# Optimization experiments

Hardware: AMD Instinct MI355X
Metric: run time of the kernel (lower is better)

Reference implementation:

```python
import jax, jax.numpy as jnp
import numpy as np

B, T, D, M = 4, 4096, 2048, 512


def setup_inputs() -> dict:
    key = jax.random.key(0)
    ks = jax.random.split(key, 6)
    x = jax.random.normal(ks[0], (B, T, D), dtype=jnp.float32)
    memory_state = jnp.zeros((B, M), dtype=jnp.float32)
    # xavier_normal-style init for the linear layers, zero biases
    Wv = jax.random.normal(ks[1], (M, D), dtype=jnp.float32) * np.float32(np.sqrt(2.0 / (D + M)))
    bv = jnp.zeros((M,), dtype=jnp.float32)
    Wg = jax.random.normal(ks[2], (D, D + M), dtype=jnp.float32) * np.float32(np.sqrt(2.0 / (2 * D + M)))
    bg = jnp.zeros((D,), dtype=jnp.float32)
    time_decay = jax.random.normal(ks[3], (M,), dtype=jnp.float32) * 0.01
    time_first = jax.random.normal(ks[4], (M,), dtype=jnp.float32) * 0.01
    return dict(x=x, memory_state=memory_state, Wv=Wv, bv=bv, Wg=Wg, bg=bg,
                time_decay=time_decay, time_first=time_first)


def reference(x, memory_state, Wv, bv, Wg, bg, time_decay, time_first):
    # v = value_proj(x): [B, T, M]
    v = jnp.einsum('btd,md->btm', x, Wv) + bv
    decay = jax.nn.sigmoid(time_decay) * 0.9 + 0.1   # [M]
    first = jax.nn.sigmoid(time_first)               # [M]

    # Recurrence: s_0 = memory_state; wv_t = v_t + s_t*first; s_{t+1} = s_t*decay + v_t
    def step(s, v_t):
        wv_t = v_t + s * first
        return s * decay + v_t, wv_t

    v_tb = jnp.swapaxes(v, 0, 1)                     # [T, B, M] for scan over time
    next_memory, wv_tb = jax.lax.scan(step, memory_state, v_tb)
    weighted_values = jnp.swapaxes(wv_tb, 0, 1)      # [B, T, M]

    # output = x + output_gate(concat[x, weighted_values])
    combined = jnp.concatenate([x, weighted_values], axis=-1)  # [B, T, D+M]
    output = x + jnp.einsum('btk,dk->btd', combined, Wg) + bg
    return output, next_memory
```

## Files before the change

kernel.cpp:

```cpp
#include <hip/hip_runtime.h>
#include <hip/hip_bf16.h>
#include <cstdint>
#include <cstddef>

#define B_DIM 4
#define T_DIM 4096
#define D_DIM 2048
#define M_DIM 512
#define NTOK  (B_DIM * T_DIM)
#define KCOMB (D_DIM + M_DIM)
#define NCHUNK 64
#define CLEN   64

typedef __attribute__((ext_vector_type(8)))  __bf16 bf16x8;
typedef __attribute__((ext_vector_type(16))) float  f32x16;

__device__ __forceinline__ unsigned short f2bf(float f) {
  union { float f; unsigned u; } v; v.f = f;
  unsigned r = v.u + 0x7fffu + ((v.u >> 16) & 1u);
  return (unsigned short)(r >> 16);
}

__device__ __forceinline__ float sigmoidf(float x) { return 1.0f / (1.0f + expf(-x)); }

#define XBLK  ((NTOK * D_DIM / 4) / 256)
#define WVBLK ((M_DIM * D_DIM / 4) / 256)
#define WGBLK ((D_DIM * KCOMB / 4) / 256)
__global__ void cast_all_kernel(const float* __restrict__ x, const float* __restrict__ Wv,
                                const float* __restrict__ Wg,
                                unsigned short* __restrict__ comb,
                                unsigned short* __restrict__ WvB,
                                unsigned short* __restrict__ WgB) {
  int bid = blockIdx.x;
  const float* src; unsigned short* dst; size_t soff, doff;
  if (bid < XBLK) {
    int idx = bid * 256 + threadIdx.x;
    int n = idx >> 9;
    int c = (idx & 511) << 2;
    src = x;   soff = (size_t)n * D_DIM + c;
    dst = comb; doff = (size_t)n * KCOMB + c;
  } else if (bid < XBLK + WVBLK) {
    int idx = (bid - XBLK) * 256 + threadIdx.x;
    src = Wv;  soff = (size_t)idx * 4;
    dst = WvB; doff = (size_t)idx * 4;
  } else {
    int idx = (bid - XBLK - WVBLK) * 256 + threadIdx.x;
    src = Wg;  soff = (size_t)idx * 4;
    dst = WgB; doff = (size_t)idx * 4;
  }
  float4 v = *(const float4*)(src + soff);
  ushort4 o;
  o.x = f2bf(v.x); o.y = f2bf(v.y); o.z = f2bf(v.z); o.w = f2bf(v.w);
  *(ushort4*)(dst + doff) = o;
}

__global__ __launch_bounds__(M_DIM) void recur_partial(
    const float* __restrict__ v, const float* __restrict__ td, float* __restrict__ P) {
  int m = threadIdx.x;
  int b = blockIdx.x >> 6;
  int c = blockIdx.x & (NCHUNK - 1);
  float decay = sigmoidf(td[m]) * 0.9f + 0.1f;
  const float* vp = v + ((size_t)(b * T_DIM + c * CLEN)) * M_DIM + m;
  float p = 0.0f;
  for (int t0 = 0; t0 < CLEN; t0 += 8) {
    float vt[8];
#pragma unroll
    for (int u = 0; u < 8; ++u) vt[u] = vp[(size_t)(t0 + u) * M_DIM];
#pragma unroll
    for (int u = 0; u < 8; ++u) p = p * decay + vt[u];
  }
  P[(size_t)blockIdx.x * M_DIM + m] = p;
}

__global__ __launch_bounds__(M_DIM) void recur_apply(
    const float* __restrict__ v, const float* __restrict__ mem0,
    const float* __restrict__ td, const float* __restrict__ tf,
    const float* __restrict__ P,
    unsigned short* __restrict__ comb, float* __restrict__ nmem) {
  int m = threadIdx.x;
  int b = blockIdx.x >> 6;
  int c = blockIdx.x & (NCHUNK - 1);
  float decay = sigmoidf(td[m]) * 0.9f + 0.1f;
  float first = sigmoidf(tf[m]);
  float dL = decay;
  dL = dL * dL; dL = dL * dL; dL = dL * dL; dL = dL * dL; dL = dL * dL; dL = dL * dL;

  float s = mem0[b * M_DIM + m];
  const float* Pp = P + (size_t)(b * NCHUNK) * M_DIM + m;
  for (int ci = 0; ci < c; ++ci)
    s = s * dL + Pp[(size_t)ci * M_DIM];

  const float* vp = v + ((size_t)(b * T_DIM + c * CLEN)) * M_DIM + m;
  unsigned short* wp = comb + ((size_t)(b * T_DIM + c * CLEN)) * KCOMB + D_DIM + m;
  for (int t0 = 0; t0 < CLEN; t0 += 8) {
    float vt[8];
#pragma unroll
    for (int u = 0; u < 8; ++u) vt[u] = vp[(size_t)(t0 + u) * M_DIM];
#pragma unroll
    for (int u = 0; u < 8; ++u) {
      wp[(size_t)(t0 + u) * KCOMB] = f2bf(vt[u] + s * first);
      s = s * decay + vt[u];
    }
  }
  if (c == NCHUNK - 1) nmem[b * M_DIM + m] = s;
}

#define BM 128
#define BN 128
#define BK 64

template <bool ADD_X, int MODE>
__global__ __launch_bounds__(256) void gemm_bt(
    const unsigned short* __restrict__ A, int lda,
    const unsigned short* __restrict__ B, int ldb,
    const float* __restrict__ bias, const float* __restrict__ xadd,
    float* __restrict__ C, int N, int K) {
  const int tid = threadIdx.x;
  const int lane = tid & 63;
  const int wave = tid >> 6;
  const int wm = (wave >> 1) * 64;
  const int wn = (wave & 1) * 64;
  const int l31 = lane & 31;
  const int half = lane >> 5;

  int tileM, tileN;
  {
    int idx = blockIdx.x;
    int xcd = idx & 7, local = idx >> 3;
    if (MODE == 1) {
      tileN = (xcd * 2 + (local & 1)) * BN;
      tileM = (local >> 1) * BM;
    } else {
      tileM = (xcd * 16 + (local >> 2)) * BM;
      tileN = (local & 3) * BN;
    }
  }

  __shared__ unsigned short As[BM * BK];
  __shared__ unsigned short Bs[BN * BK];

  f32x16 acc[2][2] = {};

  for (int k0 = 0; k0 < K; k0 += BK) {
#pragma unroll
    for (int j = 0; j < 4; ++j) {
      int c = j * 256 + tid;
      int row = c >> 3;
      int kc = c & 7;
      int gkc = kc ^ (row & 7);
      const unsigned short* gA = A + (size_t)(tileM + row) * lda + k0 + gkc * 8;
      const unsigned short* gB = B + (size_t)(tileN + row) * ldb + k0 + gkc * 8;
      __builtin_amdgcn_global_load_lds((const __attribute__((address_space(1))) void*)gA,
                                       (__attribute__((address_space(3))) void*)(As + c * 8),
                                       16, 0, 0);
      __builtin_amdgcn_global_load_lds((const __attribute__((address_space(1))) void*)gB,
                                       (__attribute__((address_space(3))) void*)(Bs + c * 8),
                                       16, 0, 0);
    }
    __syncthreads();

#pragma unroll
    for (int s = 0; s < 4; ++s) {
      const int g = s * 2 + half;
      bf16x8 af[2], bfr[2];
#pragma unroll
      for (int i = 0; i < 2; ++i) {
        int ra = wm + i * 32 + l31;
        int rb = wn + i * 32 + l31;
        af[i]  = *(const bf16x8*)(As + ra * BK + ((g ^ (ra & 7)) * 8));
        bfr[i] = *(const bf16x8*)(Bs + rb * BK + ((g ^ (rb & 7)) * 8));
      }
#pragma unroll
      for (int mi = 0; mi < 2; ++mi)
#pragma unroll
        for (int ni = 0; ni < 2; ++ni)
          acc[mi][ni] = __builtin_amdgcn_mfma_f32_32x32x16_bf16(af[mi], bfr[ni], acc[mi][ni], 0, 0, 0);
    }
    __syncthreads();
  }

#pragma unroll
  for (int mi = 0; mi < 2; ++mi) {
#pragma unroll
    for (int ni = 0; ni < 2; ++ni) {
      int col = tileN + wn + ni * 32 + l31;
      float bcol = bias[col];
#pragma unroll
      for (int r = 0; r < 16; ++r) {
        int row = tileM + wm + mi * 32 + 4 * half + (r & 3) + 8 * (r >> 2);
        float val = acc[mi][ni][r] + bcol;
        if (ADD_X) val += xadd[(size_t)row * N + col];
        C[(size_t)row * N + col] = val;
      }
    }
  }
}

#define BAR_FENCE() do { asm volatile("" ::: "memory"); \
  __builtin_amdgcn_s_barrier(); asm volatile("" ::: "memory"); } while (0)

template <bool ADD_X, int LDA, int LDB, int NOUT, int KTOT>
__global__ __launch_bounds__(512, 2) void gemm256_bt(
    const unsigned short* __restrict__ Amat,
    const unsigned short* __restrict__ Bmat,
    const float* __restrict__ bias,
    const float* __restrict__ xadd,
    float* __restrict__ C) {
  constexpr int NK  = KTOT / 64;
  constexpr int NI  = NK / 2;
  constexpr int NTN = NOUT / 256;
  constexpr int NWG = (NTOK / 256) * NTN;
  constexpr int PERX = NWG / 8;

  __shared__ unsigned short As[2][256 * 64];
  __shared__ unsigned short Bs[2][256 * 64];

  const int tid  = threadIdx.x;
  const int lane = tid & 63;
  const int half = lane >> 5;
  const int l31  = lane & 31;
  const int wave = tid >> 6;
  const int wrow = (wave >> 2) * 128;
  const int wcol = (wave & 3) * 64;

  const int bid   = blockIdx.x;
  const int wgid  = (bid & 7) * PERX + (bid >> 3);
  const int tileM = (wgid / NTN) * 256;
  const int tileN = (wgid % NTN) * 256;

  const int row_lo = tid >> 3;
  const int scol   = (((tid & 7) ^ (row_lo & 7)) << 3);
  const unsigned short* pA = Amat + (size_t)(tileM + row_lo) * LDA + scol;
  const unsigned short* pB = Bmat + (size_t)(tileN + row_lo) * LDB + scol;

#define STAGE_A(b, h, kt) do { \
  _Pragma("unroll") for (int j = 0; j < 2; ++j) { \
    const unsigned short* _s = pA + (size_t)((h) * 128 + j * 64) * LDA + (kt) * 64; \
    __builtin_amdgcn_global_load_lds((const __attribute__((address_space(1))) void*)_s, \
        (__attribute__((address_space(3))) void*)(&As[(b)][(h) * 8192 + (j * 512 + tid) * 8]), \
        16, 0, 0); \
  } \
} while (0)

#define STAGE_B(b, h, kt) do { \
  _Pragma("unroll") for (int j = 0; j < 2; ++j) { \
    const unsigned short* _s = pB + (size_t)((h) * 128 + j * 64) * LDB + (kt) * 64; \
    __builtin_amdgcn_global_load_lds((const __attribute__((address_space(1))) void*)_s, \
        (__attribute__((address_space(3))) void*)(&Bs[(b)][(h) * 8192 + (j * 512 + tid) * 8]), \
        16, 0, 0); \
  } \
} while (0)

  f32x16 acc[4][2] = {};
  bf16x8 af[2][4];
  bf16x8 bfr[4];

#define READ_A(b, mh) do { \
  _Pragma("unroll") for (int mi = 0; mi < 2; ++mi) { \
    const int _r = wrow + (mh) * 64 + mi * 32 + l31; \
    _Pragma("unroll") for (int s = 0; s < 4; ++s) \
      af[mi][s] = *(const bf16x8*)(&As[(b)][_r * 64 + (((s * 2 + half) ^ (_r & 7)) << 3)]); \
  } \
} while (0)

#define READ_B(b, ni) do { \
  const int _r = wcol + (ni) * 32 + l31; \
  _Pragma("unroll") for (int s = 0; s < 4; ++s) \
    bfr[s] = *(const bf16x8*)(&Bs[(b)][_r * 64 + (((s * 2 + half) ^ (_r & 7)) << 3)]); \
} while (0)

#define MFMA_QUAD(mh, ni) do { \
  _Pragma("unroll") for (int s = 0; s < 4; ++s) \
    _Pragma("unroll") for (int mi = 0; mi < 2; ++mi) \
      acc[(mh) * 2 + mi][(ni)] = __builtin_amdgcn_mfma_f32_32x32x16_bf16( \
          af[mi][s], bfr[s], acc[(mh) * 2 + mi][(ni)], 0, 0, 0); \
} while (0)

#define PHASE_TAIL(mh, ni) do { \
  BAR_FENCE(); \
  asm volatile("s_waitcnt lgkmcnt(0)" ::: "memory"); \
  __builtin_amdgcn_s_setprio(1); \
  MFMA_QUAD(mh, ni); \
  __builtin_amdgcn_s_setprio(0); \
  BAR_FENCE(); \
} while (0)

  STAGE_A(0, 0, 0);
  STAGE_A(0, 1, 0);
  STAGE_B(0, 0, 0);
  STAGE_B(0, 1, 0);
  STAGE_A(1, 0, 1);
  asm volatile("s_waitcnt vmcnt(2)" ::: "memory");
  BAR_FENCE();

#define ITER8(KE, FULL) do { \
   \
  READ_A(0, 0); READ_B(0, 0); \
  STAGE_A(1, 1, (KE) + 1); \
  asm volatile("s_waitcnt lgkmcnt(8)" ::: "memory"); \
  PHASE_TAIL(0, 0); \
   \
  READ_B(0, 1); \
  STAGE_B(1, 0, (KE) + 1); \
  PHASE_TAIL(0, 1); \
   \
  READ_A(0, 1); \
  STAGE_B(1, 1, (KE) + 1); \
  PHASE_TAIL(1, 1); \
   \
  READ_B(0, 0); \
  if (FULL) { STAGE_A(0, 0, (KE) + 2); \
              asm volatile("s_waitcnt vmcnt(2)" ::: "memory"); } \
  else      { asm volatile("s_waitcnt vmcnt(0)" ::: "memory"); } \
  PHASE_TAIL(1, 0); \
   \
  READ_A(1, 0); READ_B(1, 0); \
  if (FULL) STAGE_A(0, 1, (KE) + 2); \
  asm volatile("s_waitcnt lgkmcnt(8)" ::: "memory"); \
  PHASE_TAIL(0, 0); \
   \
  READ_B(1, 1); \
  if (FULL) STAGE_B(0, 0, (KE) + 2); \
  PHASE_TAIL(0, 1); \
   \
  READ_A(1, 1); \
  if (FULL) STAGE_B(0, 1, (KE) + 2); \
  PHASE_TAIL(1, 1); \
   \
  READ_B(1, 0); \
  if (FULL) { STAGE_A(1, 0, (KE) + 3); \
              asm volatile("s_waitcnt vmcnt(2)" ::: "memory"); } \
  PHASE_TAIL(1, 0); \
} while (0)

#pragma unroll 1
  for (int i = 0; i < NI - 1; ++i) ITER8(2 * i, 1);
  ITER8(2 * (NI - 1), 0);

#undef ITER8
#undef PHASE_TAIL
#undef MFMA_QUAD
#undef READ_B
#undef READ_A
#undef STAGE_B
#undef STAGE_A

#pragma unroll
  for (int mq = 0; mq < 4; ++mq) {
#pragma unroll
    for (int ni = 0; ni < 2; ++ni) {
      const int col = tileN + wcol + ni * 32 + l31;
      const float bc = bias[col];
#pragma unroll
      for (int r = 0; r < 16; ++r) {
        const int row = tileM + wrow + mq * 32 + 4 * half + (r & 3) + 8 * (r >> 2);
        float val = acc[mq][ni][r] + bc;
        if (ADD_X) val += xadd[(size_t)row * NOUT + col];
        C[(size_t)row * NOUT + col] = val;
      }
    }
  }
}

extern "C" void kernel_launch(void* const* d_in, const int* in_sizes, int n_in,
                              void* d_out, int out_size, void* d_ws, size_t ws_size,
                              hipStream_t stream) {
  const float* x   = (const float*)d_in[0];
  const float* mem = (const float*)d_in[1];
  const float* Wv  = (const float*)d_in[2];
  const float* bv  = (const float*)d_in[3];
  const float* Wg  = (const float*)d_in[4];
  const float* bg  = (const float*)d_in[5];
  const float* td  = (const float*)d_in[6];
  const float* tf  = (const float*)d_in[7];
  float* out = (float*)d_out;

  char* ws = (char*)d_ws;
  unsigned short* comb = (unsigned short*)ws;
  float* v = (float*)(ws + (size_t)NTOK * KCOMB * 2);
  unsigned short* WvB = (unsigned short*)((char*)v + (size_t)NTOK * M_DIM * 4);
  unsigned short* WgB = (unsigned short*)((char*)WvB + (size_t)M_DIM * D_DIM * 2);
  float* P = (float*)WvB;

  cast_all_kernel<<<XBLK + WVBLK + WGBLK, 256, 0, stream>>>(x, Wv, Wg, comb, WvB, WgB);

  gemm_bt<false, 0><<<(NTOK / BM) * (M_DIM / BN), 256, 0, stream>>>(
      comb, KCOMB, WvB, D_DIM, bv, nullptr, v, M_DIM, D_DIM);

  recur_partial<<<B_DIM * NCHUNK, M_DIM, 0, stream>>>(v, td, P);
  recur_apply<<<B_DIM * NCHUNK, M_DIM, 0, stream>>>(
      v, mem, td, tf, P, comb, out + (size_t)NTOK * D_DIM);

  gemm256_bt<true, KCOMB, KCOMB, D_DIM, KCOMB>
      <<<(NTOK / 256) * (D_DIM / 256), 512, 0, stream>>>(comb, WgB, bg, x, out);
}
```

Baseline: 512.3 us.

## Split B fragments by k-subslice and restage global loads in pairs

Restructures the GEMM main loop so each phase reads B fragments for both N sub-tiles over half the K slice, and runs MFMAs across mi×ni rather than over the full K for one ni. Global-to-LDS staging is regrouped so that whole A or B buffers are issued together, with vmcnt thresholds adjusted to match. A sched_barrier is added before the MFMA block. The aim is better interleaving of LDS reads, global loads and MFMA issue. The risk is a mismatch between the new staging order and the waits, or extra register pressure.

```diff
diff --git a/kernel.cpp b/kernel.cpp
--- a/kernel.cpp
+++ b/kernel.cpp
@@ -253,7 +253,7 @@
 
   f32x16 acc[4][2] = {};
   bf16x8 af[2][4];
-  bf16x8 bfr[4];
+  bf16x8 bfr[2][2];
 
 #define READ_A(b, mh) do { \
   _Pragma("unroll") for (int mi = 0; mi < 2; ++mi) { \
@@ -263,84 +263,81 @@
   } \
 } while (0)
 
-#define READ_B(b, ni) do { \
-  const int _r = wcol + (ni) * 32 + l31; \
-  _Pragma("unroll") for (int s = 0; s < 4; ++s) \
-    bfr[s] = *(const bf16x8*)(&Bs[(b)][_r * 64 + (((s * 2 + half) ^ (_r & 7)) << 3)]); \
-} while (0)
-
-#define MFMA_QUAD(mh, ni) do { \
-  _Pragma("unroll") for (int s = 0; s < 4; ++s) \
+#define READ_BSP(b, sp) do { \
+  _Pragma("unroll") for (int ni = 0; ni < 2; ++ni) { \
+    const int _r = wcol + ni * 32 + l31; \
+    _Pragma("unroll") for (int j = 0; j < 2; ++j) \
+      bfr[ni][j] = *(const bf16x8*)(&Bs[(b)][_r * 64 + \
+          (((((sp) * 2 + j) * 2 + half) ^ (_r & 7)) << 3)]); \
+  } \
+} while (0)
+
+#define MFMA_Q(mh, sp) do { \
+  _Pragma("unroll") for (int j = 0; j < 2; ++j) \
     _Pragma("unroll") for (int mi = 0; mi < 2; ++mi) \
-      acc[(mh) * 2 + mi][(ni)] = __builtin_amdgcn_mfma_f32_32x32x16_bf16( \
-          af[mi][s], bfr[s], acc[(mh) * 2 + mi][(ni)], 0, 0, 0); \
-} while (0)
-
-#define PHASE_TAIL(mh, ni) do { \
+      _Pragma("unroll") for (int ni = 0; ni < 2; ++ni) \
+        acc[(mh) * 2 + mi][(ni)] = __builtin_amdgcn_mfma_f32_32x32x16_bf16( \
+            af[mi][(sp) * 2 + j], bfr[ni][j], acc[(mh) * 2 + mi][(ni)], 0, 0, 0); \
+} while (0)
+
+#define PHASE_TAIL(mh, sp) do { \
   BAR_FENCE(); \
   asm volatile("s_waitcnt lgkmcnt(0)" ::: "memory"); \
+  __builtin_amdgcn_sched_barrier(0); \
   __builtin_amdgcn_s_setprio(1); \
-  MFMA_QUAD(mh, ni); \
+  MFMA_Q(mh, sp); \
   __builtin_amdgcn_s_setprio(0); \
   BAR_FENCE(); \
 } while (0)
 
-  STAGE_A(0, 0, 0);
-  STAGE_A(0, 1, 0);
-  STAGE_B(0, 0, 0);
-  STAGE_B(0, 1, 0);
-  STAGE_A(1, 0, 1);
-  asm volatile("s_waitcnt vmcnt(2)" ::: "memory");
+  STAGE_A(0, 0, 0); STAGE_A(0, 1, 0);
+  STAGE_B(0, 0, 0); STAGE_B(0, 1, 0);
+  STAGE_A(1, 0, 1); STAGE_A(1, 1, 1);
+  asm volatile("s_waitcnt vmcnt(4)" ::: "memory");
   BAR_FENCE();
 
-#define ITER8(KE, FULL) do { \
-   \
-  READ_A(0, 0); READ_B(0, 0); \
-  STAGE_A(1, 1, (KE) + 1); \
-  asm volatile("s_waitcnt lgkmcnt(8)" ::: "memory"); \
+#define ITER(i2, FULL) do { \
+   \
+  READ_A(0, 0); READ_BSP(0, 0); \
+  STAGE_B(1, 0, (i2) + 1); STAGE_B(1, 1, (i2) + 1); \
   PHASE_TAIL(0, 0); \
    \
-  READ_B(0, 1); \
-  STAGE_B(1, 0, (KE) + 1); \
+  READ_BSP(0, 1); \
   PHASE_TAIL(0, 1); \
    \
   READ_A(0, 1); \
-  STAGE_B(1, 1, (KE) + 1); \
   PHASE_TAIL(1, 1); \
    \
-  READ_B(0, 0); \
-  if (FULL) { STAGE_A(0, 0, (KE) + 2); \
-              asm volatile("s_waitcnt vmcnt(2)" ::: "memory"); } \
+  READ_BSP(0, 0); \
+  if (FULL) { STAGE_A(0, 0, (i2) + 2); STAGE_A(0, 1, (i2) + 2); \
+              asm volatile("s_waitcnt vmcnt(4)" ::: "memory"); } \
   else      { asm volatile("s_waitcnt vmcnt(0)" ::: "memory"); } \
   PHASE_TAIL(1, 0); \
    \
-  READ_A(1, 0); READ_B(1, 0); \
-  if (FULL) STAGE_A(0, 1, (KE) + 2); \
-  asm volatile("s_waitcnt lgkmcnt(8)" ::: "memory"); \
+  READ_A(1, 0); READ_BSP(1, 0); \
+  if (FULL) { STAGE_B(0, 0, (i2) + 2); STAGE_B(0, 1, (i2) + 2); } \
   PHASE_TAIL(0, 0); \
    \
-  READ_B(1, 1); \
-  if (FULL) STAGE_B(0, 0, (KE) + 2); \
+  READ_BSP(1, 1); \
   PHASE_TAIL(0, 1); \
    \
   READ_A(1, 1); \
-  if (FULL) STAGE_B(0, 1, (KE) + 2); \
   PHASE_TAIL(1, 1); \
    \
-  READ_B(1, 0); \
-  if (FULL) { STAGE_A(1, 0, (KE) + 3); \
-              asm volatile("s_waitcnt vmcnt(2)" ::: "memory"); } \
+  READ_BSP(1, 0); \
+  if (FULL) { STAGE_A(1, 0, (i2) + 3); STAGE_A(1, 1, (i2) + 3); \
+              asm volatile("s_waitcnt vmcnt(4)" ::: "memory"); } \
   PHASE_TAIL(1, 0); \
 } while (0)
 
 #pragma unroll 1
-  for (int i = 0; i < NI - 1; ++i) ITER8(2 * i, 1);
-  ITER8(2 * (NI - 1), 0);
-
-#undef ITER8
+  for (int i = 0; i < NI - 1; ++i) ITER(2 * i, 1);
+  ITER(2 * (NI - 1), 0);
+
+#undef ITER
 #undef PHASE_TAIL
-#undef MFMA_QUAD
-#undef READ_B
+#undef MFMA_Q
+#undef READ_BSP
 #undef READ_A
 #undef STAGE_B
 #undef STAGE_A
```

Result: no change. 508.7 us (-0.7%).
